# Kernel optimization log

Hardware: AMD Instinct MI355X
Metric: run time of the kernel (lower is better)

Reference implementation:

```python
import jax, jax.numpy as jnp
import numpy as np

GRID = (192, 96, 192)
NUM_MATERIALS = 8
WORLD_SCALE = 2.0
OCC_THRESHOLD = 0.01
TEMPERATURE = 1.0


def _look_at(eye, target, up):
    eye = np.asarray(eye, np.float32); target = np.asarray(target, np.float32); up = np.asarray(up, np.float32)
    f = target - eye; f = f / np.linalg.norm(f)
    r = np.cross(f, up); r = r / np.linalg.norm(r)
    u = np.cross(r, f)
    view = np.eye(4, dtype=np.float32)
    view[0, :3] = r;  view[0, 3] = -r @ eye
    view[1, :3] = u;  view[1, 3] = -u @ eye
    view[2, :3] = -f; view[2, 3] = f @ eye
    return view


def _perspective(fov_deg, aspect, near, far):
    f = 1.0 / np.tan(np.radians(fov_deg) / 2.0)
    p = np.zeros((4, 4), dtype=np.float32)
    p[0, 0] = f / aspect
    p[1, 1] = f
    p[2, 2] = (far + near) / (near - far)
    p[2, 3] = 2.0 * far * near / (near - far)
    p[3, 2] = -1.0
    return p


def setup_inputs() -> dict:
    key = jax.random.key(0)
    k1, k2 = jax.random.split(key)
    X, Y, Z = GRID
    occupancy_logits = jax.random.normal(k1, (X, Y, Z), dtype=jnp.float32)
    material_logits = jax.random.normal(k2, (X, Y, Z, NUM_MATERIALS), dtype=jnp.float32)
    # grid world extent: x,z in [-X/2, X/2]*scale, y in [0, Y]*scale
    camera_view = jnp.asarray(_look_at(eye=(0.0, 250.0, 700.0), target=(0.0, 96.0, 0.0), up=(0.0, 1.0, 0.0)))
    camera_proj = jnp.asarray(_perspective(60.0, 1.0, 0.1, 2000.0))
    return {
        'occupancy_logits': occupancy_logits,
        'material_logits': material_logits,
        'camera_view': camera_view,
        'camera_proj': camera_proj,
        'max_blocks': 100000,
    }


def _voxel_centers(X, Y, Z):
    # centers = (idx + 0.5 + offset) * world_scale, offset = (-X/2, 0, -Z/2)
    cx = (jnp.arange(X, dtype=jnp.float32) + 0.5 - X / 2.0) * WORLD_SCALE
    cy = (jnp.arange(Y, dtype=jnp.float32) + 0.5) * WORLD_SCALE
    cz = (jnp.arange(Z, dtype=jnp.float32) + 0.5 - Z / 2.0) * WORLD_SCALE
    gx, gy, gz = jnp.meshgrid(cx, cy, cz, indexing='ij')
    return jnp.stack([gx.ravel(), gy.ravel(), gz.ravel()], axis=-1)  # (N, 3)


def reference(occupancy_logits, material_logits, camera_view, camera_proj, max_blocks):
    X, Y, Z = occupancy_logits.shape
    N = X * Y * Z
    occ = jax.nn.sigmoid(occupancy_logits).reshape(-1)          # (N,)
    active = occ > OCC_THRESHOLD                                # torch.nonzero -> mask

    centers = _voxel_centers(X, Y, Z)                           # (N, 3) world centers

    # frustum test in NDC (world_to_clip with combined MVP)
    mvp = camera_proj @ camera_view                             # (4, 4)
    clip = centers @ mvp[:, :3].T + mvp[:, 3]                   # (N, 4)
    w = jnp.maximum(clip[:, 3], 1e-6)
    ndc = clip[:, :3] / w[:, None]
    visible = jnp.all((ndc >= -1.0) & (ndc <= 1.0), axis=-1)

    valid = active & visible

    # depth-based top-k: keep max_blocks nearest valid voxels
    view_z = centers @ camera_view[2, :3] + camera_view[2, 3]
    depth = jnp.maximum(-view_z, 0.0)
    score = jnp.where(valid, -depth, -jnp.inf)                  # nearest first
    _, idx = jax.lax.top_k(score, max_blocks)
    keep = jnp.zeros((N,), dtype=bool).at[idx].set(valid[idx])  # pruned_mask scatter

    pruned_weights = jnp.where(keep, occ, 0.0).reshape(X, Y, Z)

    # render prep: per-voxel material distribution scaled by occupancy weight
    mat_probs = jax.nn.softmax(material_logits / TEMPERATURE, axis=-1)
    return pruned_weights[..., None] * mat_probs                # (X, Y, Z, M)
```

## Files before the change

### kernel.cpp

```cpp
#include <hip/hip_runtime.h>

#define GX 192
#define GY 96
#define GZ 192
#define GRP (GY*GZ)
#define NVOX (GX*GRP)

#define NXC 3
#define XCW (GX/NXC)
#define GBLK (GRP/256)

#define K2T 1024
#define GPT (GRP/K2T)
#define WBINS 4096
#define BPT (WBINS/K2T)

#define WS_MVP    0
#define WS_DEPTH  64
#define WS_CNT3   (WS_DEPTH + GRP*4)
#define WS_SEL    (WS_CNT3 + NXC*GRP*4)
#define WS_TLIST  (WS_SEL + 16)
#define WS_TPREF  (WS_TLIST + 1024)
#define WS_NTIED  (WS_TPREF + GX*4)

__device__ __forceinline__ bool voxel_valid(int x, int g,
                                            const float* __restrict__ occL,
                                            const float* M,
                                            float* occ_out)
{
    int y = g / GZ;
    int z = g - y * GZ;
    float cx = (float)(2 * x - 191);
    float cy = (float)(2 * y + 1);
    float cz = (float)(2 * z - 191);

    float logit = occL[(size_t)x * GRP + g];
    float occ = 1.0f / (1.0f + expf(-logit));
    *occ_out = occ;
    if (!(occ > 0.01f)) return false;

    float c0 = __fadd_rn(__fmaf_rn(cz, M[2],  __fmaf_rn(cy, M[1],  __fmul_rn(cx, M[0]))),  M[3]);
    float c1 = __fadd_rn(__fmaf_rn(cz, M[6],  __fmaf_rn(cy, M[5],  __fmul_rn(cx, M[4]))),  M[7]);
    float c2 = __fadd_rn(__fmaf_rn(cz, M[10], __fmaf_rn(cy, M[9],  __fmul_rn(cx, M[8]))),  M[11]);
    float c3 = __fadd_rn(__fmaf_rn(cz, M[14], __fmaf_rn(cy, M[13], __fmul_rn(cx, M[12]))), M[15]);

    float w  = fmaxf(c3, 1e-6f);
    float nx = c0 / w;
    float ny = c1 / w;
    float nz = c2 / w;
    return (nx >= -1.0f) && (nx <= 1.0f) &&
           (ny >= -1.0f) && (ny <= 1.0f) &&
           (nz >= -1.0f) && (nz <= 1.0f);
}

__device__ __forceinline__ void compute_mvp_lds(const float* view, const float* proj,
                                                float* s_mvp, int tid)
{
    if (tid < 16) {
        int r = tid >> 2, c = tid & 3;
        float acc = 0.0f;
        for (int k = 0; k < 4; ++k)
            acc = __fadd_rn(acc, __fmul_rn(proj[r * 4 + k], view[k * 4 + c]));
        s_mvp[tid] = acc;
    }
}

__global__ __launch_bounds__(256) void k_prep_count(
    const float* __restrict__ view, const float* __restrict__ proj,
    const float* __restrict__ occL,
    float* __restrict__ mvpOut,
    unsigned* __restrict__ depthBits,
    unsigned* __restrict__ cnt3)
{
    __shared__ float s_mvp[16];
    int tid = threadIdx.x;
    compute_mvp_lds(view, proj, s_mvp, tid);
    __syncthreads();

    int b  = blockIdx.x;
    int gb = b % GBLK;
    int xc = b / GBLK;
    int g  = gb * 256 + tid;

    if (b == 0 && tid < 16) mvpOut[tid] = s_mvp[tid];

    if (xc == 0) {
        int y = g / GZ;
        int z = g - y * GZ;
        float cy = (float)(2 * y + 1);
        float cz = (float)(2 * z - 191);
        float seed = __fmul_rn(-191.0f, view[8]);
        float vz = __fadd_rn(__fmaf_rn(cz, view[10], __fmaf_rn(cy, view[9], seed)), view[11]);
        float d  = fmaxf(-vz, 0.0f);
        depthBits[g] = __float_as_uint(d);
    }

    unsigned c = 0;
    int x0 = xc * XCW;
    for (int x = x0; x < x0 + XCW; ++x) {
        float occ;
        if (voxel_valid(x, g, occL, s_mvp, &occ)) ++c;
    }
    cnt3[(size_t)xc * GRP + g] = c;
}

__global__ __launch_bounds__(1024) void k_select(
    const float* __restrict__ view, const float* __restrict__ proj,
    const float* __restrict__ occL,
    const unsigned* __restrict__ depthBits,
    const unsigned* __restrict__ cnt3,
    const int* __restrict__ maxBlocksPtr,
    unsigned* __restrict__ sel,
    unsigned* __restrict__ tiedList,
    unsigned* __restrict__ tiedPrefX,
    unsigned* __restrict__ nTiedG)
{
    __shared__ float s_mvp[16];
    __shared__ unsigned s_h[WBINS];
    __shared__ unsigned s_scan[K2T];
    __shared__ unsigned s_wT[16], s_wMn[16], s_wMx[16];
    __shared__ unsigned s_tot, s_mn, s_mx;
    __shared__ unsigned s_found, s_prefix, s_remK;
    __shared__ unsigned s_list[256];
    __shared__ int s_n;
    __shared__ unsigned s_cntX[GX];

    int tid = threadIdx.x;
    compute_mvp_lds(view, proj, s_mvp, tid);

    unsigned d[GPT], c[GPT];
    #pragma unroll
    for (int k = 0; k < GPT; ++k) {
        int g = tid + k * K2T;
        d[k] = depthBits[g];
        c[k] = cnt3[g] + cnt3[GRP + g] + cnt3[2 * GRP + g];
    }

    unsigned tot = 0, mn = 0xFFFFFFFFu, mx = 0;
    #pragma unroll
    for (int k = 0; k < GPT; ++k) {
        tot += c[k];
        if (c[k]) {
            unsigned hi = d[k] >> 16;
            mn = min(mn, hi);
            mx = max(mx, hi);
        }
    }
    for (int m = 1; m < 64; m <<= 1) {
        tot += (unsigned)__shfl_xor((int)tot, m);
        mn = min(mn, (unsigned)__shfl_xor((int)mn, m));
        mx = max(mx, (unsigned)__shfl_xor((int)mx, m));
    }
    int wid = tid >> 6;
    if ((tid & 63) == 0) { s_wT[wid] = tot; s_wMn[wid] = mn; s_wMx[wid] = mx; }
    __syncthreads();
    if (tid == 0) {
        unsigned t2 = 0, m2 = 0xFFFFFFFFu, x2 = 0;
        for (int w = 0; w < 16; ++w) {
            t2 += s_wT[w]; m2 = min(m2, s_wMn[w]); x2 = max(x2, s_wMx[w]);
        }
        s_tot = t2; s_mn = m2; s_mx = x2;
        s_found = 0;
    }
    __syncthreads();
    unsigned K = (unsigned)maxBlocksPtr[0];
    tot = s_tot; mn = s_mn; mx = s_mx;

    if (tot <= K) {
        if (tid == 0) {
            sel[0] = 0xFFFFFFFFu;
            sel[1] = 0x7FFFFFFFu;
            *nTiedG = 0u;
        }
        return;
    }

    unsigned remK = K;
    unsigned prefix = 0;
    unsigned span = mx - mn + 1u;
    unsigned nchunks = (span + WBINS - 1u) / WBINS;
    for (unsigned ch = 0; ch < nchunks; ++ch) {
        unsigned base = mn + ch * WBINS;
        #pragma unroll
        for (int j = 0; j < BPT; ++j) s_h[tid + j * K2T] = 0;
        __syncthreads();
        #pragma unroll
        for (int k = 0; k < GPT; ++k) {
            if (c[k]) {
                unsigned hi = d[k] >> 16;
                if (hi >= base && hi < base + WBINS)
                    atomicAdd(&s_h[hi - base], c[k]);
            }
        }
        __syncthreads();
        unsigned ps = 0;
        #pragma unroll
        for (int j = 0; j < BPT; ++j) ps += s_h[tid * BPT + j];
        s_scan[tid] = ps;
        __syncthreads();
        for (int off = 1; off < K2T; off <<= 1) {
            unsigned v = s_scan[tid];
            unsigned a = (tid >= off) ? s_scan[tid - off] : 0u;
            __syncthreads();
            s_scan[tid] = v + a;
            __syncthreads();
        }
        unsigned incl = s_scan[tid];
        unsigned chunkTot = s_scan[K2T - 1];
        unsigned excl = incl - ps;
        if (remK <= chunkTot && excl < remK && remK <= incl) {
            unsigned cum = excl;
            #pragma unroll
            for (int j = 0; j < BPT; ++j) {
                unsigned hv = s_h[tid * BPT + j];
                if (cum < remK && remK <= cum + hv) {
                    s_found  = 1u;
                    s_prefix = base + (unsigned)(tid * BPT + j);
                    s_remK   = remK - cum;
                }
                cum += hv;
            }
        }
        __syncthreads();
        if (s_found) { prefix = s_prefix; remK = s_remK; break; }
        remK -= chunkTot;
        __syncthreads();
    }

    for (int p = 0; p < 2; ++p) {
        int matchShift = (p == 0) ? 16 : 8;
        int digitShift = (p == 0) ? 8 : 0;
        if (tid < 256) s_h[tid] = 0;
        __syncthreads();
        #pragma unroll
        for (int k = 0; k < GPT; ++k) {
            if (c[k] && (d[k] >> matchShift) == prefix)
                atomicAdd(&s_h[(d[k] >> digitShift) & 255u], c[k]);
        }
        __syncthreads();
        unsigned ps = (tid < 256) ? s_h[tid] : 0u;
        s_scan[tid] = ps;
        __syncthreads();
        for (int off = 1; off < K2T; off <<= 1) {
            unsigned v = s_scan[tid];
            unsigned a = (tid >= off) ? s_scan[tid - off] : 0u;
            __syncthreads();
            s_scan[tid] = v + a;
            __syncthreads();
        }
        unsigned incl = s_scan[tid];
        unsigned excl = incl - ps;
        if (excl < remK && remK <= incl) {
            s_prefix = (prefix << 8) | (unsigned)tid;
            s_remK   = remK - excl;
        }
        __syncthreads();
        prefix = s_prefix; remK = s_remK;
        __syncthreads();
    }
    unsigned T = prefix;
    unsigned R = remK;

    if (tid == 0) s_n = 0;
    for (int x = tid; x < GX; x += K2T) s_cntX[x] = 0;
    __syncthreads();
    #pragma unroll
    for (int k = 0; k < GPT; ++k) {
        if (d[k] == T) {
            int idx = atomicAdd(&s_n, 1);
            if (idx < 256) s_list[idx] = (unsigned)(tid + k * K2T);
        }
    }
    __syncthreads();
    int n = min(s_n, 256);
    if (tid == 0) {
        for (int a = 1; a < n; ++a) {
            unsigned v = s_list[a];
            int b = a - 1;
            while (b >= 0 && s_list[b] > v) { s_list[b + 1] = s_list[b]; --b; }
            s_list[b + 1] = v;
        }
    }
    __syncthreads();
    int pairs = GX * n;
    for (int pr = tid; pr < pairs; pr += K2T) {
        int x = pr / n;
        int s = pr - x * n;
        float occ;
        if (voxel_valid(x, (int)s_list[s], occL, s_mvp, &occ))
            atomicAdd(&s_cntX[x], 1u);
    }
    __syncthreads();
    if (tid == 0) {
        unsigned run = 0;
        for (int x = 0; x < GX; ++x) { tiedPrefX[x] = run; run += s_cntX[x]; }
        *nTiedG = (unsigned)n;
        sel[0] = T;
        sel[1] = R;
    }
    if (tid < n) tiedList[tid] = s_list[tid];
}

__global__ void k_out(const float* __restrict__ occL,
                      const float* __restrict__ matL,
                      const float* __restrict__ mvp,
                      const unsigned* __restrict__ depthBits,
                      const unsigned* __restrict__ sel,
                      const unsigned* __restrict__ tiedList,
                      const unsigned* __restrict__ tiedPrefX,
                      const unsigned* __restrict__ nTiedPtr,
                      float* __restrict__ out)
{
    int i = blockIdx.x * 256 + threadIdx.x;
    if (i >= NVOX) return;
    int x = i / GRP;
    int g = i - x * GRP;

    float occ;
    bool valid = voxel_valid(x, g, occL, mvp, &occ);
    bool keep = false;
    if (valid) {
        unsigned T  = sel[0];
        unsigned db = depthBits[g];
        if (db < T) {
            keep = true;
        } else if (db == T) {
            unsigned R = sel[1];
            unsigned rank = tiedPrefX[x];
            int n = (int)*nTiedPtr;
            for (int s = 0; s < n; ++s) {
                unsigned gs = tiedList[s];
                if (gs >= (unsigned)g) break;
                float o2;
                if (voxel_valid(x, (int)gs, occL, mvp, &o2)) ++rank;
            }
            keep = rank < R;
        }
    }

    float4 o0 = make_float4(0.f, 0.f, 0.f, 0.f);
    float4 o1 = make_float4(0.f, 0.f, 0.f, 0.f);
    if (keep) {
        const float4* mp = reinterpret_cast<const float4*>(matL) + (size_t)i * 2;
        float4 a = mp[0];
        float4 b = mp[1];
        float mx = fmaxf(fmaxf(fmaxf(a.x, a.y), fmaxf(a.z, a.w)),
                         fmaxf(fmaxf(b.x, b.y), fmaxf(b.z, b.w)));
        float e0 = expf(a.x - mx), e1 = expf(a.y - mx), e2 = expf(a.z - mx), e3 = expf(a.w - mx);
        float e4 = expf(b.x - mx), e5 = expf(b.y - mx), e6 = expf(b.z - mx), e7 = expf(b.w - mx);
        float s = ((e0 + e1) + (e2 + e3)) + ((e4 + e5) + (e6 + e7));
        float inv = occ / s;
        o0 = make_float4(e0 * inv, e1 * inv, e2 * inv, e3 * inv);
        o1 = make_float4(e4 * inv, e5 * inv, e6 * inv, e7 * inv);
    }
    float4* op = reinterpret_cast<float4*>(out) + (size_t)i * 2;
    op[0] = o0;
    op[1] = o1;
}

extern "C" void kernel_launch(void* const* d_in, const int* in_sizes, int n_in,
                              void* d_out, int out_size, void* d_ws, size_t ws_size,
                              hipStream_t stream)
{
    const float* occL = (const float*)d_in[0];
    const float* matL = (const float*)d_in[1];
    const float* view = (const float*)d_in[2];
    const float* proj = (const float*)d_in[3];
    const int*   mb   = (const int*)d_in[4];

    char* ws = (char*)d_ws;
    float*    mvp      = (float*)(ws + WS_MVP);
    unsigned* depthB   = (unsigned*)(ws + WS_DEPTH);
    unsigned* cnt3     = (unsigned*)(ws + WS_CNT3);
    unsigned* sel      = (unsigned*)(ws + WS_SEL);
    unsigned* tiedList = (unsigned*)(ws + WS_TLIST);
    unsigned* tiedPref = (unsigned*)(ws + WS_TPREF);
    unsigned* nTied    = (unsigned*)(ws + WS_NTIED);

    k_prep_count<<<NXC * GBLK, 256, 0, stream>>>(view, proj, occL, mvp, depthB, cnt3);
    k_select<<<1, K2T, 0, stream>>>(view, proj, occL, depthB, cnt3, mb,
                                    sel, tiedList, tiedPref, nTied);
    k_out<<<NVOX / 256, 256, 0, stream>>>(occL, matL, mvp, depthB, sel,
                                          tiedList, tiedPref, nTied, (float*)d_out);
}
```

Before: 77.79 us.

## Split count pass finer, pack byte counts, use wave-shuffle scans, nontemporal output

The count kernel's x-axis split goes from 3 to 12 chunks, so it launches more blocks. Per-chunk counts are stored as bytes in a 16-byte stride, so the select kernel sums them with three 32-bit loads. The 1024-thread LDS Hillis-Steele scans in the single-block select kernel become a wave-shuffle scan plus a 16-wave combine, which removes about 20 barriers per scan. The output kernel uses nontemporal loads and stores for the material logits and the result, to reduce cache pollution on streaming data.

```diff
diff --git a/kernel.cpp b/kernel.cpp
--- a/kernel.cpp
+++ b/kernel.cpp
@@ -6,9 +6,10 @@
 #define GRP (GY*GZ)
 #define NVOX (GX*GRP)
 
-#define NXC 3
+#define NXC 12
 #define XCW (GX/NXC)
 #define GBLK (GRP/256)
+#define CSTR 16
 
 #define K2T 1024
 #define GPT (GRP/K2T)
@@ -17,11 +18,13 @@
 
 #define WS_MVP    0
 #define WS_DEPTH  64
-#define WS_CNT3   (WS_DEPTH + GRP*4)
-#define WS_SEL    (WS_CNT3 + NXC*GRP*4)
+#define WS_CNT8   (WS_DEPTH + GRP*4)
+#define WS_SEL    (WS_CNT8 + GRP*CSTR)
 #define WS_TLIST  (WS_SEL + 16)
 #define WS_TPREF  (WS_TLIST + 1024)
 #define WS_NTIED  (WS_TPREF + GX*4)
+
+typedef float f4 __attribute__((ext_vector_type(4)));
 
 __device__ __forceinline__ bool voxel_valid(int x, int g,
                                             const float* __restrict__ occL,
@@ -65,12 +68,22 @@
     }
 }
 
+__device__ __forceinline__ unsigned wave_incl_scan(unsigned v, int lane)
+{
+    #pragma unroll
+    for (int off = 1; off < 64; off <<= 1) {
+        unsigned u = (unsigned)__shfl_up((int)v, off);
+        if (lane >= off) v += u;
+    }
+    return v;
+}
+
 __global__ __launch_bounds__(256) void k_prep_count(
     const float* __restrict__ view, const float* __restrict__ proj,
     const float* __restrict__ occL,
     float* __restrict__ mvpOut,
     unsigned* __restrict__ depthBits,
-    unsigned* __restrict__ cnt3)
+    unsigned char* __restrict__ cnt8)
 {
     __shared__ float s_mvp[16];
     int tid = threadIdx.x;
@@ -101,14 +114,14 @@
         float occ;
         if (voxel_valid(x, g, occL, s_mvp, &occ)) ++c;
     }
-    cnt3[(size_t)xc * GRP + g] = c;
+    cnt8[(size_t)g * CSTR + xc] = (unsigned char)c;
 }
 
 __global__ __launch_bounds__(1024) void k_select(
     const float* __restrict__ view, const float* __restrict__ proj,
     const float* __restrict__ occL,
     const unsigned* __restrict__ depthBits,
-    const unsigned* __restrict__ cnt3,
+    const unsigned char* __restrict__ cnt8,
     const int* __restrict__ maxBlocksPtr,
     unsigned* __restrict__ sel,
     unsigned* __restrict__ tiedList,
@@ -117,15 +130,17 @@
 {
     __shared__ float s_mvp[16];
     __shared__ unsigned s_h[WBINS];
-    __shared__ unsigned s_scan[K2T];
+    __shared__ unsigned s_w[16];
     __shared__ unsigned s_wT[16], s_wMn[16], s_wMx[16];
-    __shared__ unsigned s_tot, s_mn, s_mx;
+    __shared__ unsigned s_tot, s_mn, s_mx, s_chTot;
     __shared__ unsigned s_found, s_prefix, s_remK;
     __shared__ unsigned s_list[256];
     __shared__ int s_n;
     __shared__ unsigned s_cntX[GX];
 
-    int tid = threadIdx.x;
+    int tid  = threadIdx.x;
+    int lane = tid & 63;
+    int wid  = tid >> 6;
     compute_mvp_lds(view, proj, s_mvp, tid);
 
     unsigned d[GPT], c[GPT];
@@ -133,7 +148,12 @@
     for (int k = 0; k < GPT; ++k) {
         int g = tid + k * K2T;
         d[k] = depthBits[g];
-        c[k] = cnt3[g] + cnt3[GRP + g] + cnt3[2 * GRP + g];
+        const unsigned* cp = (const unsigned*)(cnt8 + (size_t)g * CSTR);
+        unsigned w0 = cp[0], w1 = cp[1], w2 = cp[2];
+        unsigned s = (w0 & 255u) + ((w0 >> 8) & 255u) + ((w0 >> 16) & 255u) + (w0 >> 24);
+        s += (w1 & 255u) + ((w1 >> 8) & 255u) + ((w1 >> 16) & 255u) + (w1 >> 24);
+        s += (w2 & 255u) + ((w2 >> 8) & 255u) + ((w2 >> 16) & 255u) + (w2 >> 24);
+        c[k] = s;
     }
 
     unsigned tot = 0, mn = 0xFFFFFFFFu, mx = 0;
@@ -151,8 +171,7 @@
         mn = min(mn, (unsigned)__shfl_xor((int)mn, m));
         mx = max(mx, (unsigned)__shfl_xor((int)mx, m));
     }
-    int wid = tid >> 6;
-    if ((tid & 63) == 0) { s_wT[wid] = tot; s_wMn[wid] = mn; s_wMx[wid] = mx; }
+    if (lane == 0) { s_wT[wid] = tot; s_wMn[wid] = mn; s_wMx[wid] = mx; }
     __syncthreads();
     if (tid == 0) {
         unsigned t2 = 0, m2 = 0xFFFFFFFFu, x2 = 0;
@@ -196,17 +215,18 @@
         unsigned ps = 0;
         #pragma unroll
         for (int j = 0; j < BPT; ++j) ps += s_h[tid * BPT + j];
-        s_scan[tid] = ps;
-        __syncthreads();
-        for (int off = 1; off < K2T; off <<= 1) {
-            unsigned v = s_scan[tid];
-            unsigned a = (tid >= off) ? s_scan[tid - off] : 0u;
-            __syncthreads();
-            s_scan[tid] = v + a;
-            __syncthreads();
-        }
-        unsigned incl = s_scan[tid];
-        unsigned chunkTot = s_scan[K2T - 1];
+        unsigned iw = wave_incl_scan(ps, lane);
+        if (lane == 63) s_w[wid] = iw;
+        __syncthreads();
+        if (wid == 0) {
+            unsigned wv = (lane < 16) ? s_w[lane] : 0u;
+            unsigned wiw = wave_incl_scan(wv, lane);
+            if (lane < 16) s_w[lane] = wiw - wv;
+            if (lane == 15) s_chTot = wiw;
+        }
+        __syncthreads();
+        unsigned incl = iw + s_w[wid];
+        unsigned chunkTot = s_chTot;
         unsigned excl = incl - ps;
         if (remK <= chunkTot && excl < remK && remK <= incl) {
             unsigned cum = excl;
@@ -239,16 +259,16 @@
         }
         __syncthreads();
         unsigned ps = (tid < 256) ? s_h[tid] : 0u;
-        s_scan[tid] = ps;
-        __syncthreads();
-        for (int off = 1; off < K2T; off <<= 1) {
-            unsigned v = s_scan[tid];
-            unsigned a = (tid >= off) ? s_scan[tid - off] : 0u;
-            __syncthreads();
-            s_scan[tid] = v + a;
-            __syncthreads();
-        }
-        unsigned incl = s_scan[tid];
+        unsigned iw = wave_incl_scan(ps, lane);
+        if (lane == 63) s_w[wid] = iw;
+        __syncthreads();
+        if (wid == 0) {
+            unsigned wv = (lane < 16) ? s_w[lane] : 0u;
+            unsigned wiw = wave_incl_scan(wv, lane);
+            if (lane < 16) s_w[lane] = wiw - wv;
+        }
+        __syncthreads();
+        unsigned incl = iw + s_w[wid];
         unsigned excl = incl - ps;
         if (excl < remK && remK <= incl) {
             s_prefix = (prefix << 8) | (unsigned)tid;
@@ -301,15 +321,16 @@
     if (tid < n) tiedList[tid] = s_list[tid];
 }
 
-__global__ void k_out(const float* __restrict__ occL,
-                      const float* __restrict__ matL,
-                      const float* __restrict__ mvp,
-                      const unsigned* __restrict__ depthBits,
-                      const unsigned* __restrict__ sel,
-                      const unsigned* __restrict__ tiedList,
-                      const unsigned* __restrict__ tiedPrefX,
-                      const unsigned* __restrict__ nTiedPtr,
-                      float* __restrict__ out)
+__global__ __launch_bounds__(256) void k_out(
+    const float* __restrict__ occL,
+    const float* __restrict__ matL,
+    const float* __restrict__ mvp,
+    const unsigned* __restrict__ depthBits,
+    const unsigned* __restrict__ sel,
+    const unsigned* __restrict__ tiedList,
+    const unsigned* __restrict__ tiedPrefX,
+    const unsigned* __restrict__ nTiedPtr,
+    float* __restrict__ out)
 {
     int i = blockIdx.x * 256 + threadIdx.x;
     if (i >= NVOX) return;
@@ -338,24 +359,24 @@
         }
     }
 
-    float4 o0 = make_float4(0.f, 0.f, 0.f, 0.f);
-    float4 o1 = make_float4(0.f, 0.f, 0.f, 0.f);
+    f4 o0 = (f4)(0.0f);
+    f4 o1 = (f4)(0.0f);
     if (keep) {
-        const float4* mp = reinterpret_cast<const float4*>(matL) + (size_t)i * 2;
-        float4 a = mp[0];
-        float4 b = mp[1];
-        float mx = fmaxf(fmaxf(fmaxf(a.x, a.y), fmaxf(a.z, a.w)),
-                         fmaxf(fmaxf(b.x, b.y), fmaxf(b.z, b.w)));
-        float e0 = expf(a.x - mx), e1 = expf(a.y - mx), e2 = expf(a.z - mx), e3 = expf(a.w - mx);
-        float e4 = expf(b.x - mx), e5 = expf(b.y - mx), e6 = expf(b.z - mx), e7 = expf(b.w - mx);
+        const f4* mp = reinterpret_cast<const f4*>(matL) + (size_t)i * 2;
+        f4 a = __builtin_nontemporal_load(mp);
+        f4 b = __builtin_nontemporal_load(mp + 1);
+        float mx = fmaxf(fmaxf(fmaxf(a[0], a[1]), fmaxf(a[2], a[3])),
+                         fmaxf(fmaxf(b[0], b[1]), fmaxf(b[2], b[3])));
+        float e0 = expf(a[0] - mx), e1 = expf(a[1] - mx), e2 = expf(a[2] - mx), e3 = expf(a[3] - mx);
+        float e4 = expf(b[0] - mx), e5 = expf(b[1] - mx), e6 = expf(b[2] - mx), e7 = expf(b[3] - mx);
         float s = ((e0 + e1) + (e2 + e3)) + ((e4 + e5) + (e6 + e7));
         float inv = occ / s;
-        o0 = make_float4(e0 * inv, e1 * inv, e2 * inv, e3 * inv);
-        o1 = make_float4(e4 * inv, e5 * inv, e6 * inv, e7 * inv);
-    }
-    float4* op = reinterpret_cast<float4*>(out) + (size_t)i * 2;
-    op[0] = o0;
-    op[1] = o1;
+        o0[0] = e0 * inv; o0[1] = e1 * inv; o0[2] = e2 * inv; o0[3] = e3 * inv;
+        o1[0] = e4 * inv; o1[1] = e5 * inv; o1[2] = e6 * inv; o1[3] = e7 * inv;
+    }
+    f4* op = reinterpret_cast<f4*>(out) + (size_t)i * 2;
+    __builtin_nontemporal_store(o0, op);
+    __builtin_nontemporal_store(o1, op + 1);
 }
 
 extern "C" void kernel_launch(void* const* d_in, const int* in_sizes, int n_in,
@@ -369,16 +390,16 @@
     const int*   mb   = (const int*)d_in[4];
 
     char* ws = (char*)d_ws;
-    float*    mvp      = (float*)(ws + WS_MVP);
-    unsigned* depthB   = (unsigned*)(ws + WS_DEPTH);
-    unsigned* cnt3     = (unsigned*)(ws + WS_CNT3);
-    unsigned* sel      = (unsigned*)(ws + WS_SEL);
-    unsigned* tiedList = (unsigned*)(ws + WS_TLIST);
-    unsigned* tiedPref = (unsigned*)(ws + WS_TPREF);
-    unsigned* nTied    = (unsigned*)(ws + WS_NTIED);
-
-    k_prep_count<<<NXC * GBLK, 256, 0, stream>>>(view, proj, occL, mvp, depthB, cnt3);
-    k_select<<<1, K2T, 0, stream>>>(view, proj, occL, depthB, cnt3, mb,
+    float*         mvp      = (float*)(ws + WS_MVP);
+    unsigned*      depthB   = (unsigned*)(ws + WS_DEPTH);
+    unsigned char* cnt8     = (unsigned char*)(ws + WS_CNT8);
+    unsigned*      sel      = (unsigned*)(ws + WS_SEL);
+    unsigned*      tiedList = (unsigned*)(ws + WS_TLIST);
+    unsigned*      tiedPref = (unsigned*)(ws + WS_TPREF);
+    unsigned*      nTied    = (unsigned*)(ws + WS_NTIED);
+
+    k_prep_count<<<NXC * GBLK, 256, 0, stream>>>(view, proj, occL, mvp, depthB, cnt8);
+    k_select<<<1, K2T, 0, stream>>>(view, proj, occL, depthB, cnt8, mb,
                                     sel, tiedList, tiedPref, nTied);
     k_out<<<NVOX / 256, 256, 0, stream>>>(occL, matL, mvp, depthB, sel,
                                           tiedList, tiedPref, nTied, (float*)d_out);
```

Result: faster. 64.11 us (-17.6%).
